# Performance work log

Hardware: AMD Instinct MI355X
Metric: run time of the kernel (lower is better)

The kernel has to match this reference:

```python
import jax, jax.numpy as jnp
import numpy as np

B, T, D = 2, 2048, 2048
H, KV = 16, 4
HD = D // H  # 128
ROPE_BASE = 10000.0


def _rope(t):
    # t: [B, h, T, HD]; faithful to torch apply_rope (even/odd split, concat halves)
    pos = jnp.arange(T, dtype=t.dtype)
    inv_freq = 1.0 / (ROPE_BASE ** (jnp.arange(0, HD, 2, dtype=t.dtype) / HD))
    ang = jnp.einsum('t,f->tf', pos, inv_freq)  # [T, HD/2]
    sin = jnp.sin(ang)[None, None]
    cos = jnp.cos(ang)[None, None]
    t1, t2 = t[..., ::2], t[..., 1::2]
    return jnp.concatenate([t1 * cos - t2 * sin, t1 * sin + t2 * cos], axis=-1)


def setup_inputs() -> dict:
    key = jax.random.key(0)
    kx, kq, kk, kv, ko = jax.random.split(key, 5)
    x = jax.random.normal(kx, (B, T, D), dtype=jnp.float32)
    s = 0.02
    Wq = jax.random.normal(kq, (D, D), dtype=jnp.float32) * s
    Wk = jax.random.normal(kk, (D, KV * HD), dtype=jnp.float32) * s
    Wv = jax.random.normal(kv, (D, KV * HD), dtype=jnp.float32) * s
    Wo = jax.random.normal(ko, (D, D), dtype=jnp.float32) * s
    return {"x": x, "Wq": Wq, "Wk": Wk, "Wv": Wv, "Wo": Wo}


def reference(x, Wq, Wk, Wv, Wo):
    # projections (nn.Linear, no bias)
    q = (x @ Wq).reshape(B, T, H, HD).transpose(0, 2, 1, 3)    # [B,H,T,HD]
    k = (x @ Wk).reshape(B, T, KV, HD).transpose(0, 2, 1, 3)   # [B,KV,T,HD]
    v = (x @ Wv).reshape(B, T, KV, HD).transpose(0, 2, 1, 3)
    q = _rope(q)
    k = _rope(k)
    # GQA: repeat_interleave kv heads to full head count
    g = H // KV
    k = jnp.repeat(k, g, axis=1)
    v = jnp.repeat(v, g, axis=1)
    # causal SDPA, default scale 1/sqrt(head_dim)
    scale = 1.0 / jnp.sqrt(jnp.array(HD, dtype=x.dtype))
    scores = jnp.einsum('bhqd,bhkd->bhqk', q, k) * scale
    mask = jnp.tril(jnp.ones((T, T), dtype=bool))
    scores = jnp.where(mask, scores, jnp.finfo(scores.dtype).min)
    attn = jax.nn.softmax(scores, axis=-1)
    out = jnp.einsum('bhqk,bhkd->bhqd', attn, v)               # [B,H,T,HD]
    out = out.transpose(0, 2, 1, 3).reshape(B, T, D)
    return out @ Wo
```

## Files before the change

kernel.cpp:

```cpp
#include <hip/hip_runtime.h>
#include <math.h>

#define BB 2
#define TT 2048
#define DD 2048
#define HH 16
#define KVHN 4
#define HDIM 128
#define NKV 3072

typedef unsigned short u16;
typedef unsigned int u32;
typedef __bf16 bf16x8 __attribute__((ext_vector_type(8)));
typedef float  f32x4  __attribute__((ext_vector_type(4)));

#define AS1 __attribute__((address_space(1)))
#define AS3 __attribute__((address_space(3)))

__device__ __forceinline__ void dma16(const u16* g, u16* l) {
  __builtin_amdgcn_global_load_lds((const AS1 u32*)g, (AS3 u32*)l, 16, 0, 0);
}

__device__ __forceinline__ u16 f2bf(float f) {
  u32 u = __float_as_uint(f);
  u32 r = (u + 0x7FFFu + ((u >> 16) & 1u)) >> 16;
  return (u16)r;
}
__device__ __forceinline__ float bf2f(u32 h) { return __uint_as_float(h << 16); }

__device__ __forceinline__ u32 pack2(float a, float b) {
  union { __bf16 h[2]; u32 u; } cv;
  cv.h[0] = (__bf16)a; cv.h[1] = (__bf16)b;
  return cv.u;
}

__global__ __launch_bounds__(256) void castf2b(const float* __restrict__ in,
                                               u16* __restrict__ out) {
  size_t i4 = (size_t)blockIdx.x * 256 + threadIdx.x;
  float4 v = *(const float4*)(in + i4 * 4);
  ushort4 o;
  o.x = f2bf(v.x); o.y = f2bf(v.y); o.z = f2bf(v.z); o.w = f2bf(v.w);
  *(ushort4*)(out + i4 * 4) = o;
}

__global__ __launch_bounds__(256) void tcast(const float* __restrict__ W,
                                             u16* __restrict__ WT,
                                             int K, int N) {
  __shared__ float tile[32][33];
  const int n0 = blockIdx.x * 32, k0 = blockIdx.y * 32;
  const int r = threadIdx.x >> 3;
  const int c4 = (threadIdx.x & 7) * 4;
  float4 v = *(const float4*)(W + (size_t)(k0 + r) * N + n0 + c4);
  tile[r][c4 + 0] = v.x; tile[r][c4 + 1] = v.y;
  tile[r][c4 + 2] = v.z; tile[r][c4 + 3] = v.w;
  __syncthreads();
  ushort4 o;
  o.x = f2bf(tile[c4 + 0][r]); o.y = f2bf(tile[c4 + 1][r]);
  o.z = f2bf(tile[c4 + 2][r]); o.w = f2bf(tile[c4 + 3][r]);
  *(ushort4*)(WT + (size_t)(n0 + r) * K + k0 + c4) = o;
}

template <int OUT_BF16>
__global__ __launch_bounds__(256) void gemm2(const u16* __restrict__ A,
                                             const u16* __restrict__ BT,
                                             void* __restrict__ Cv,
                                             int N, int K) {
  __shared__ u16 As[128 * 32];
  __shared__ u16 Bs[128 * 32];
  const int t = threadIdx.x;
  const int l = t & 63, w = t >> 6;
  const int lm = l & 15, quad = l >> 4;
  const int wm = w & 1, wn = w >> 1;
  const int m0 = blockIdx.y * 128, n0 = blockIdx.x * 128;
  const int wu = __builtin_amdgcn_readfirstlane(w);

  f32x4 acc[4][4];
  #pragma unroll
  for (int i = 0; i < 4; ++i)
    #pragma unroll
    for (int j = 0; j < 4; ++j) acc[i][j] = (f32x4){0.f, 0.f, 0.f, 0.f};

  for (int k0 = 0; k0 < K; k0 += 32) {
    __syncthreads();
    #pragma unroll
    for (int i = 0; i < 2; ++i) {
      int p0 = (wu * 2 + i) * 64;
      int p = p0 + l;
      int row = p >> 2, c = p & 3;
      dma16(A  + (size_t)(m0 + row) * K + k0 + c * 8, &As[p0 * 8]);
      dma16(BT + (size_t)(n0 + row) * K + k0 + c * 8, &Bs[p0 * 8]);
    }
    __syncthreads();
    bf16x8 a[4], bq[4];
    #pragma unroll
    for (int i = 0; i < 4; ++i)
      a[i] = *(const bf16x8*)&As[(wm * 64 + i * 16 + lm) * 32 + quad * 8];
    #pragma unroll
    for (int j = 0; j < 4; ++j)
      bq[j] = *(const bf16x8*)&Bs[(wn * 64 + j * 16 + lm) * 32 + quad * 8];
    #pragma unroll
    for (int i = 0; i < 4; ++i)
      #pragma unroll
      for (int j = 0; j < 4; ++j)
        acc[i][j] = __builtin_amdgcn_mfma_f32_16x16x32_bf16(a[i], bq[j], acc[i][j], 0, 0, 0);
  }

  #pragma unroll
  for (int i = 0; i < 4; ++i) {
    #pragma unroll
    for (int r = 0; r < 4; ++r) {
      size_t gr = (size_t)(m0 + wm * 64 + i * 16 + quad * 4 + r);
      #pragma unroll
      for (int j = 0; j < 4; ++j) {
        int gc = n0 + wn * 64 + j * 16 + lm;
        if (OUT_BF16) ((u16*)Cv)[gr * N + gc] = f2bf(acc[i][j][r]);
        else          ((float*)Cv)[gr * N + gc] = acc[i][j][r];
      }
    }
  }
}

__global__ __launch_bounds__(256) void rope2(u16* p) {
  const int row = blockIdx.x;
  const int pos = row & (TT - 1);
  u16* base = p + (size_t)row * NKV;
  float e0[5], e1[5];
  #pragma unroll
  for (int i = 0; i < 5; ++i) {
    int item = threadIdx.x + i * 256;
    int h20 = item >> 6, f = item & 63;
    int col = (h20 < 16) ? h20 * 128 : 2048 + (h20 - 16) * 128;
    u32 u = *(const u32*)(base + col + 2 * f);
    e0[i] = bf2f(u & 0xffffu);
    e1[i] = bf2f(u >> 16);
  }
  __syncthreads();
  #pragma unroll
  for (int i = 0; i < 5; ++i) {
    int item = threadIdx.x + i * 256;
    int h20 = item >> 6, f = item & 63;
    int col = (h20 < 16) ? h20 * 128 : 2048 + (h20 - 16) * 128;
    float sc = (h20 < 16) ? 0.08838834764831845f : 1.0f;
    float inv = exp2f((float)f * -0.20762050593046898f);
    float ang = (float)pos * inv;
    float sn, cs;
    sincosf(ang, &sn, &cs);
    base[col + f]      = f2bf((e0[i] * cs - e1[i] * sn) * sc);
    base[col + 64 + f] = f2bf((e0[i] * sn + e1[i] * cs) * sc);
  }
}

__global__ __launch_bounds__(256) void vtrans(const u16* __restrict__ QKV,
                                              u16* __restrict__ Vt) {
  __shared__ u16 tl[64][72];
  const int t0 = blockIdx.x * 64;
  const int y  = blockIdx.y;
  const int b  = blockIdx.z;
  #pragma unroll
  for (int i = 0; i < 2; ++i) {
    int idx = threadIdx.x + i * 256;
    int r = idx >> 3, c = (idx & 7) * 8;
    *(uint4*)&tl[r][c] =
        *(const uint4*)(QKV + (size_t)(b * TT + t0 + r) * NKV + 2560 + y * 64 + c);
  }
  __syncthreads();
  const int vh = y >> 1;
  #pragma unroll
  for (int i = 0; i < 2; ++i) {
    int idx = threadIdx.x + i * 256;
    int dr = idx >> 3, tc = (idx & 7) * 8;
    u16 tmp[8];
    #pragma unroll
    for (int j = 0; j < 8; ++j) tmp[j] = tl[tc + j][dr];
    int dloc = (y & 1) * 64 + dr;
    *(uint4*)(Vt + (size_t)((b * KVHN + vh) * HDIM + dloc) * TT + t0 + tc) =
        *(const uint4*)tmp;
  }
}

__global__ __launch_bounds__(256, 4) void attn4(const u16* __restrict__ QKV,
                                                const u16* __restrict__ Vt,
                                                u16* __restrict__ Ob) {
  __shared__ u16 KsA[32 * 128], KsB[32 * 128];
  __shared__ u16 VsA[64 * 64], VsB[64 * 64];
  __shared__ u16 Pw[4 * 512];
  const int t = threadIdx.x;
  const int l = t & 63, w = t >> 6;
  const int lm = l & 15, quad = l >> 4;
  const int h = blockIdx.y, b = blockIdx.z;
  const int qbase = (blockIdx.x + (blockIdx.y & 7)) & 31;
  const int qt = (blockIdx.y & 8) ? (31 - qbase) : qbase;
  const int kvh = h >> 2;
  const int q0 = qt * 64;
  const int last = 2 * qt + 1;
  const int wu = __builtin_amdgcn_readfirstlane(w);
  u16* pwv = &Pw[w * 512];
  constexpr float L2E = 1.4426950408889634f;

  bf16x8 qf[4];
  {
    size_t r0 = (size_t)(b * TT + q0 + w * 16 + lm) * NKV + h * HDIM;
    #pragma unroll
    for (int ks = 0; ks < 4; ++ks)
      qf[ks] = *(const bf16x8*)(QKV + r0 + ks * 32 + quad * 8);
  }

  f32x4 o[8];
  #pragma unroll
  for (int i = 0; i < 8; ++i) o[i] = (f32x4){0.f, 0.f, 0.f, 0.f};
  float m_ = -1e30f, l_ = 0.f;

  const u16 *kg[2], *vg[2];
  int koff[2], voff[2];
  #pragma unroll
  for (int i = 0; i < 2; ++i) {
    int p0 = (wu * 2 + i) * 64, p = p0 + l;
    int krow = p >> 4, kcp = p & 15, kcl = kcp ^ (krow & 15);
    kg[i] = QKV + (size_t)(b * TT + krow) * NKV + 2048 + kvh * HDIM + kcl * 8;
    koff[i] = p0 * 8;
    int vrow = p >> 3, vphys = p & 7, vcl = vphys ^ (vrow & 7);
    int vd = vrow + (vcl >> 2) * 64, vtch = vcl & 3;
    vg[i] = Vt + (size_t)((b * KVHN + kvh) * HDIM + vd) * TT + vtch * 8;
    voff[i] = p0 * 8;
  }

  #pragma unroll
  for (int i = 0; i < 2; ++i) {
    dma16(kg[i], KsA + koff[i]);
    dma16(vg[i], VsA + voff[i]);
    kg[i] += 32 * NKV;
    vg[i] += 32;
  }

  const int qrow = q0 + w * 16 + lm;

  auto body = [&](int kt, const u16* kcur, const u16* vcur, u16* knx, u16* vnx) {
    __syncthreads();
    const bool pf = kt < last;
    if (pf) {
      #pragma unroll
      for (int i = 0; i < 2; ++i) dma16(vg[i], vnx + voff[i]);
    }

    f32x4 s[2];
    s[0] = (f32x4){0.f, 0.f, 0.f, 0.f};
    s[1] = (f32x4){0.f, 0.f, 0.f, 0.f};
    __builtin_amdgcn_s_setprio(1);
    #pragma unroll
    for (int ks = 0; ks < 4; ++ks) {
      #pragma unroll
      for (int mt = 0; mt < 2; ++mt) {
        bf16x8 kb = *(const bf16x8*)&kcur[(mt * 16 + lm) * 128 + (((ks * 4 + quad) ^ lm) * 8)];
        s[mt] = __builtin_amdgcn_mfma_f32_16x16x32_bf16(kb, qf[ks], s[mt], 0, 0, 0);
      }
    }
    __builtin_amdgcn_s_setprio(0);
    if (pf) {
      #pragma unroll
      for (int i = 0; i < 2; ++i) {
        dma16(kg[i], knx + koff[i]);
        kg[i] += 32 * NKV;
        vg[i] += 32;
      }
    }

    if (kt >= 2 * qt) {
      #pragma unroll
      for (int mt = 0; mt < 2; ++mt)
        #pragma unroll
        for (int r = 0; r < 4; ++r) {
          int kv = kt * 32 + mt * 16 + quad * 4 + r;
          if (kv > qrow) s[mt][r] = -1e30f;
        }
    }

    float mx = -1e30f;
    #pragma unroll
    for (int mt = 0; mt < 2; ++mt)
      #pragma unroll
      for (int r = 0; r < 4; ++r) mx = fmaxf(mx, s[mt][r]);
    mx = fmaxf(mx, __shfl_xor(mx, 16));
    mx = fmaxf(mx, __shfl_xor(mx, 32));
    bool upd = mx > m_ + 8.f;
    float mn = upd ? mx : m_;
    float al = upd ? exp2f((m_ - mn) * L2E) : 1.f;
    m_ = mn;
    float sum = 0.f;
    #pragma unroll
    for (int mt = 0; mt < 2; ++mt)
      #pragma unroll
      for (int r = 0; r < 4; ++r) {
        float pv = exp2f((s[mt][r] - mn) * L2E);
        s[mt][r] = pv;
        sum += pv;
      }
    sum += __shfl_xor(sum, 16);
    sum += __shfl_xor(sum, 32);
    l_ = l_ * al + sum;

    #pragma unroll
    for (int mt = 0; mt < 2; ++mt) {
      u32 p01 = pack2(s[mt][0], s[mt][1]);
      u32 p23 = pack2(s[mt][2], s[mt][3]);
      int c = mt * 2 + (quad >> 1);
      int addr = (lm >> 1) * 64 + ((lm & 1) * 4 + (c ^ ((lm >> 1) & 3))) * 8 + (quad & 1) * 4;
      uint2 uv; uv.x = p01; uv.y = p23;
      *(uint2*)&pwv[addr] = uv;
    }
    if (__any(upd)) {
      #pragma unroll
      for (int i = 0; i < 8; ++i)
        #pragma unroll
        for (int r = 0; r < 4; ++r) o[i][r] *= al;
    }

    int paddr = (lm >> 1) * 64 + ((lm & 1) * 4 + (quad ^ ((lm >> 1) & 3))) * 8;
    bf16x8 pb = *(const bf16x8*)&pwv[paddr];
    __builtin_amdgcn_s_setprio(1);
    #pragma unroll
    for (int mt2 = 0; mt2 < 8; ++mt2) {
      int vrow = (mt2 & 3) * 16 + lm;
      int vphys = ((mt2 >> 2) * 4 + quad) ^ (vrow & 7);
      bf16x8 vb = *(const bf16x8*)&vcur[vrow * 64 + vphys * 8];
      o[mt2] = __builtin_amdgcn_mfma_f32_16x16x32_bf16(vb, pb, o[mt2], 0, 0, 0);
    }
    __builtin_amdgcn_s_setprio(0);
  };

  for (int kt = 0; kt <= last; ++kt) {
    if ((kt & 1) == 0) body(kt, KsA, VsA, KsB, VsB);
    else               body(kt, KsB, VsB, KsA, VsA);
  }

  __syncthreads();
  u16* esc = ((w & 2) ? KsB : KsA) + (w & 1) * 2048;
  float inv = 1.f / l_;
  #pragma unroll
  for (int mt2 = 0; mt2 < 8; ++mt2) {
    u32 a0 = pack2(o[mt2][0] * inv, o[mt2][1] * inv);
    u32 a1 = pack2(o[mt2][2] * inv, o[mt2][3] * inv);
    int phys = (mt2 * 2 + (quad >> 1)) ^ (lm & 7);
    int addr = lm * 128 + phys * 8 + (quad & 1) * 4;
    uint2 uv; uv.x = a0; uv.y = a1;
    *(uint2*)&esc[addr] = uv;
  }
  #pragma unroll
  for (int i = 0; i < 4; ++i) {
    int p = i * 64 + l;
    int row = p >> 4, cl = p & 15;
    int cph = cl ^ (row & 7);
    uint4 val = *(const uint4*)&esc[row * 128 + cph * 8];
    *(uint4*)(Ob + (size_t)(b * TT + q0 + w * 16 + row) * DD + h * HDIM + cl * 8) = val;
  }
}

extern "C" void kernel_launch(void* const* d_in, const int* in_sizes, int n_in,
                              void* d_out, int out_size, void* d_ws, size_t ws_size,
                              hipStream_t stream) {
  const float* x  = (const float*)d_in[0];
  const float* Wq = (const float*)d_in[1];
  const float* Wk = (const float*)d_in[2];
  const float* Wv = (const float*)d_in[3];
  const float* Wo = (const float*)d_in[4];
  float* out = (float*)d_out;

  u16* xb    = (u16*)d_ws;
  u16* WqkvT = xb + 8388608;
  u16* WoT   = xb + 14680064;
  u16* Vt    = WqkvT;
  u16* Ob    = xb;
  u16* QKVb  = (u16*)d_out;

  dim3 blk(256);
  castf2b<<<8192, blk, 0, stream>>>(x, xb);
  tcast<<<dim3(64, 64), blk, 0, stream>>>(Wq, WqkvT, DD, DD);
  tcast<<<dim3(16, 64), blk, 0, stream>>>(Wk, WqkvT + (size_t)2048 * DD, DD, 512);
  tcast<<<dim3(16, 64), blk, 0, stream>>>(Wv, WqkvT + (size_t)2560 * DD, DD, 512);
  tcast<<<dim3(64, 64), blk, 0, stream>>>(Wo, WoT, DD, DD);

  gemm2<1><<<dim3(NKV / 128, 32), blk, 0, stream>>>(xb, WqkvT, QKVb, NKV, DD);
  rope2<<<BB * TT, blk, 0, stream>>>(QKVb);
  vtrans<<<dim3(32, 8, BB), blk, 0, stream>>>(QKVb, Vt);
  attn4<<<dim3(32, HH, BB), blk, 0, stream>>>(QKVb, Vt, Ob);
  gemm2<0><<<dim3(DD / 128, 32), blk, 0, stream>>>(Ob, WoT, out, DD, DD);
}
```

Baseline: 335.0 us.

## Replace GEMM with triple-buffered, XOR-swizzled 128x256 tile kernel using 8 waves

The projection GEMMs now use a 512-thread block computing a 128x256 tile with K-step 64. Loads go through a three-stage LDS ring with direct global-to-LDS DMA and explicit vmcnt waits, so fetching the next tiles overlaps with MFMA work. An XOR swizzle on the LDS chunk index is meant to avoid bank conflicts, and s_setprio is raised around the MFMA block. The cost is more LDS per block (about 144KB) and fewer blocks in the grid, which can lower occupancy and leave CUs idle on tail waves.

```diff
diff --git a/kernel.cpp b/kernel.cpp
--- a/kernel.cpp
+++ b/kernel.cpp
@@ -61,48 +61,85 @@
 }
 
 template <int OUT_BF16>
-__global__ __launch_bounds__(256) void gemm2(const u16* __restrict__ A,
-                                             const u16* __restrict__ BT,
-                                             void* __restrict__ Cv,
-                                             int N, int K) {
-  __shared__ u16 As[128 * 32];
-  __shared__ u16 Bs[128 * 32];
+__global__ __launch_bounds__(512) void gemm8p(const u16* __restrict__ A,
+                                              const u16* __restrict__ BT,
+                                              void* __restrict__ Cv,
+                                              int N, int K) {
+  __shared__ u16 lds[3 * 24576];
   const int t = threadIdx.x;
   const int l = t & 63, w = t >> 6;
   const int lm = l & 15, quad = l >> 4;
   const int wm = w & 1, wn = w >> 1;
-  const int m0 = blockIdx.y * 128, n0 = blockIdx.x * 128;
+  const int m0 = blockIdx.y * 128, n0 = blockIdx.x * 256;
   const int wu = __builtin_amdgcn_readfirstlane(w);
 
+  const u16* srcA[2]; int dstA[2];
+  const u16* srcB[4]; int dstB[4];
+  #pragma unroll
+  for (int i = 0; i < 2; ++i) {
+    int p0 = (wu * 2 + i) * 64, p = p0 + l;
+    int row = p >> 3, c = (p & 7) ^ (row & 7);
+    srcA[i] = A + (size_t)(m0 + row) * K + c * 8;
+    dstA[i] = p0 * 8;
+  }
+  #pragma unroll
+  for (int i = 0; i < 4; ++i) {
+    int p0 = (wu * 4 + i) * 64, p = p0 + l;
+    int row = p >> 3, c = (p & 7) ^ (row & 7);
+    srcB[i] = BT + (size_t)(n0 + row) * K + c * 8;
+    dstB[i] = 8192 + p0 * 8;
+  }
+
   f32x4 acc[4][4];
   #pragma unroll
   for (int i = 0; i < 4; ++i)
     #pragma unroll
     for (int j = 0; j < 4; ++j) acc[i][j] = (f32x4){0.f, 0.f, 0.f, 0.f};
 
-  for (int k0 = 0; k0 < K; k0 += 32) {
-    __syncthreads();
-    #pragma unroll
-    for (int i = 0; i < 2; ++i) {
-      int p0 = (wu * 2 + i) * 64;
-      int p = p0 + l;
-      int row = p >> 2, c = p & 3;
-      dma16(A  + (size_t)(m0 + row) * K + k0 + c * 8, &As[p0 * 8]);
-      dma16(BT + (size_t)(n0 + row) * K + k0 + c * 8, &Bs[p0 * 8]);
-    }
-    __syncthreads();
-    bf16x8 a[4], bq[4];
-    #pragma unroll
-    for (int i = 0; i < 4; ++i)
-      a[i] = *(const bf16x8*)&As[(wm * 64 + i * 16 + lm) * 32 + quad * 8];
-    #pragma unroll
-    for (int j = 0; j < 4; ++j)
-      bq[j] = *(const bf16x8*)&Bs[(wn * 64 + j * 16 + lm) * 32 + quad * 8];
-    #pragma unroll
-    for (int i = 0; i < 4; ++i)
+  auto stage = [&](int bsel) {
+    u16* buf = &lds[bsel * 24576];
+    #pragma unroll
+    for (int i = 0; i < 2; ++i) { dma16(srcA[i], buf + dstA[i]); srcA[i] += 64; }
+    #pragma unroll
+    for (int i = 0; i < 4; ++i) { dma16(srcB[i], buf + dstB[i]); srcB[i] += 64; }
+  };
+
+  stage(0); stage(1); stage(2);
+
+  const int NT = K >> 6;
+  int bsel = 0;
+  const int xorc = lm & 7;
+  for (int tI = 0; tI < NT; ++tI) {
+    if (tI + 2 < NT)      asm volatile("s_waitcnt vmcnt(12)" ::: "memory");
+    else if (tI + 1 < NT) asm volatile("s_waitcnt vmcnt(6)" ::: "memory");
+    else                  asm volatile("s_waitcnt vmcnt(0)" ::: "memory");
+    asm volatile("s_barrier" ::: "memory");
+
+    const u16* Ab = &lds[bsel * 24576];
+    const u16* Bb = Ab + 8192;
+    bf16x8 a[2][4], b[2][4];
+    #pragma unroll
+    for (int ks = 0; ks < 2; ++ks) {
+      int ch = ((ks * 4 + quad) ^ xorc) * 8;
+      #pragma unroll
+      for (int i = 0; i < 4; ++i)
+        a[ks][i] = *(const bf16x8*)&Ab[(wm * 64 + i * 16 + lm) * 64 + ch];
       #pragma unroll
       for (int j = 0; j < 4; ++j)
-        acc[i][j] = __builtin_amdgcn_mfma_f32_16x16x32_bf16(a[i], bq[j], acc[i][j], 0, 0, 0);
+        b[ks][j] = *(const bf16x8*)&Bb[(wn * 64 + j * 16 + lm) * 64 + ch];
+    }
+    __builtin_amdgcn_s_setprio(1);
+    #pragma unroll
+    for (int ks = 0; ks < 2; ++ks)
+      #pragma unroll
+      for (int i = 0; i < 4; ++i)
+        #pragma unroll
+        for (int j = 0; j < 4; ++j)
+          acc[i][j] = __builtin_amdgcn_mfma_f32_16x16x32_bf16(a[ks][i], b[ks][j], acc[i][j], 0, 0, 0);
+    __builtin_amdgcn_s_setprio(0);
+    asm volatile("s_barrier" ::: "memory");
+    if (tI + 3 < NT) stage(bsel);
+    bsel = (bsel == 2) ? 0 : bsel + 1;
   }
 
   #pragma unroll
@@ -378,9 +415,9 @@
   tcast<<<dim3(16, 64), blk, 0, stream>>>(Wv, WqkvT + (size_t)2560 * DD, DD, 512);
   tcast<<<dim3(64, 64), blk, 0, stream>>>(Wo, WoT, DD, DD);
 
-  gemm2<1><<<dim3(NKV / 128, 32), blk, 0, stream>>>(xb, WqkvT, QKVb, NKV, DD);
+  gemm8p<1><<<dim3(NKV / 256, 32), dim3(512), 0, stream>>>(xb, WqkvT, QKVb, NKV, DD);
   rope2<<<BB * TT, blk, 0, stream>>>(QKVb);
   vtrans<<<dim3(32, 8, BB), blk, 0, stream>>>(QKVb, Vt);
   attn4<<<dim3(32, HH, BB), blk, 0, stream>>>(QKVb, Vt, Ob);
-  gemm2<0><<<dim3(DD / 128, 32), blk, 0, stream>>>(Ob, WoT, out, DD, DD);
-}
+  gemm8p<0><<<dim3(DD / 256, 32), dim3(512), 0, stream>>>(Ob, WoT, out, DD, DD);
+}
```

New measurement: 326.4 us. 2.6% less time.
